# Kernel tuning notes

Hardware: AMD Instinct MI355X
Metric: run time of the kernel (lower is better)

Reference implementation:

```python
import jax, jax.numpy as jnp
import numpy as np

VMIN, VMAX, N = -5.0, 5.0, 100          # InvertiblePWL defaults
INT_LEN = (VMAX - VMIN) / (N - 1)       # bin width
B, D = 2_000_000, 16


def setup_inputs() -> dict:
    key = jax.random.key(0)
    k1, k2, k3, k4 = jax.random.split(key, 4)
    eps = jax.random.normal(k1, (B, D), dtype=jnp.float32)
    # small-magnitude adjacency so (I - A) is well-conditioned
    A = 0.05 * jax.random.normal(k2, (D, D), dtype=jnp.float32)
    # per-dim PWL params: torch inits p = randn(n+1)/5, b = randn(1) + vmin
    p = jax.random.normal(k3, (D, N + 1), dtype=jnp.float32) / 5.0
    b = jax.random.normal(k4, (D,), dtype=jnp.float32) + VMIN
    return {"eps": eps, "A": A, "p": p, "b": b}


def _pwl_forward(z, p, b):
    """Vectorized InvertiblePWL.forward over all d dims at once.
    z: [B, d]; p: [d, N+1]; b: [d]  ->  out: [B, d]
    """
    points = jnp.linspace(VMIN, VMAX, N, dtype=z.dtype)  # [N], same for all dims
    # delta_h is detached in torch (p[1:n] slice) -> stop_gradient
    delta_h = jax.lax.stop_gradient(INT_LEN * (jnp.exp(p[:, 1:N]) + 0.001))  # [d, N-1]
    # serial cumsum in torch == prefix-sum: delta_bias[0]=b, delta_bias[i+1]=delta_bias[i]+delta_h[i]
    delta_bias = b[:, None] + jnp.concatenate(
        [jnp.zeros((p.shape[0], 1), z.dtype), jnp.cumsum(delta_h, axis=1)], axis=1
    )  # [d, N]
    # index = sum(eps >= points) == searchsorted(points, z, 'right'), in [0, N]
    index = jnp.searchsorted(points, z, side="right")          # [B, d]
    sp_idx = jnp.maximum(index - 1, 0)                          # clamp at 0
    db = jnp.take_along_axis(delta_bias.T, sp_idx, axis=0)      # [B, d]
    sp = jax.lax.stop_gradient(points[sp_idx])                  # start points, detached
    w = jnp.exp(jnp.take_along_axis(p.T, index, axis=0)) + 0.001  # [B, d]
    return (z - sp) * w + db


def reference(eps, A, p, b):
    d = A.shape[0]
    # SCM.inv_cal: z = eps @ inv(I - A)
    adj_normalized = jnp.linalg.inv(jnp.eye(d, dtype=A.dtype) - A)
    z = eps @ adj_normalized                                    # [B, d]
    # SCM.prior_nlr: per-dim InvertiblePWL
    return _pwl_forward(z, p, b)
```

## Files before the change

kernel.cpp:

```cpp
#include <hip/hip_runtime.h>
#include <math.h>

#define D_DIM 16
#define N_PTS 100
#define VMIN_F (-5.0f)
#define INT_LEN_F (10.0f / 99.0f)
#define INV_INT_LEN_F (99.0f / 10.0f)

__global__ void scm_setup(const float* __restrict__ A,
                          const float* __restrict__ p,
                          const float* __restrict__ b,
                          float* __restrict__ Minv,
                          float* __restrict__ w_tab,
                          float* __restrict__ db) {
    __shared__ double aug[16][33];
    __shared__ int piv;
    const int t = threadIdx.x;

    if (t < 16) {
        #pragma unroll
        for (int j = 0; j < 16; j++) {
            aug[t][j]      = (t == j ? 1.0 : 0.0) - (double)A[t * 16 + j];
            aug[t][16 + j] = (t == j ? 1.0 : 0.0);
        }
    }
    __syncthreads();

    for (int k = 0; k < 16; k++) {
        if (t == 0) {
            int pr = k; double best = fabs(aug[k][k]);
            for (int i = k + 1; i < 16; i++) {
                double v = fabs(aug[i][k]);
                if (v > best) { best = v; pr = i; }
            }
            piv = pr;
        }
        __syncthreads();
        const int pr = piv;
        if (pr != k && t < 32) {
            double tmp = aug[k][t]; aug[k][t] = aug[pr][t]; aug[pr][t] = tmp;
        }
        __syncthreads();
        const double pivval = aug[k][k];
        __syncthreads();
        if (t < 32) aug[k][t] = aug[k][t] / pivval;
        __syncthreads();
        if (t < 16 && t != k) {
            const double f = aug[t][k];
            #pragma unroll
            for (int j = 0; j < 32; j++) aug[t][j] -= f * aug[k][j];
        }
        __syncthreads();
    }

    if (t < 16) {
        #pragma unroll
        for (int j = 0; j < 16; j++) Minv[t * 16 + j] = (float)aug[t][16 + j];
    }

    for (int i = t; i < 16 * (N_PTS + 1); i += blockDim.x)
        w_tab[i] = expf(p[i]) + 0.001f;

    if (t < 16) {
        float acc = b[t];
        db[t * N_PTS + 0] = acc;
        for (int i = 1; i < N_PTS; i++) {
            acc += INT_LEN_F * (expf(p[t * (N_PTS + 1) + i]) + 0.001f);
            db[t * N_PTS + i] = acc;
        }
    }
}

__global__ __launch_bounds__(256) void scm_main(
        const float* __restrict__ eps,
        const float* __restrict__ Minv,
        const float* __restrict__ w_tab,
        const float* __restrict__ db,
        float* __restrict__ out, int B) {
    __shared__ float sM[256];
    __shared__ float sW[16 * (N_PTS + 1)];
    __shared__ float sDB[16 * N_PTS];

    for (int i = threadIdx.x; i < 256; i += 256) sM[i] = Minv[i];
    for (int i = threadIdx.x; i < 16 * (N_PTS + 1); i += 256) sW[i] = w_tab[i];
    for (int i = threadIdx.x; i < 16 * N_PTS; i += 256) sDB[i] = db[i];
    __syncthreads();

    const int row = blockIdx.x * blockDim.x + threadIdx.x;
    if (row >= B) return;

    const float4* erow = (const float4*)(eps + (size_t)row * 16);
    float4 e0 = erow[0], e1 = erow[1], e2 = erow[2], e3 = erow[3];
    float e[16] = {e0.x, e0.y, e0.z, e0.w, e1.x, e1.y, e1.z, e1.w,
                   e2.x, e2.y, e2.z, e2.w, e3.x, e3.y, e3.z, e3.w};

    float z[16];
    #pragma unroll
    for (int d = 0; d < 16; d++) z[d] = 0.0f;

    #pragma unroll
    for (int k = 0; k < 16; k++) {
        const float ek = e[k];
        const float4 m0 = ((const float4*)sM)[k * 4 + 0];
        const float4 m1 = ((const float4*)sM)[k * 4 + 1];
        const float4 m2 = ((const float4*)sM)[k * 4 + 2];
        const float4 m3 = ((const float4*)sM)[k * 4 + 3];
        z[0]  = fmaf(ek, m0.x, z[0]);  z[1]  = fmaf(ek, m0.y, z[1]);
        z[2]  = fmaf(ek, m0.z, z[2]);  z[3]  = fmaf(ek, m0.w, z[3]);
        z[4]  = fmaf(ek, m1.x, z[4]);  z[5]  = fmaf(ek, m1.y, z[5]);
        z[6]  = fmaf(ek, m1.z, z[6]);  z[7]  = fmaf(ek, m1.w, z[7]);
        z[8]  = fmaf(ek, m2.x, z[8]);  z[9]  = fmaf(ek, m2.y, z[9]);
        z[10] = fmaf(ek, m2.z, z[10]); z[11] = fmaf(ek, m2.w, z[11]);
        z[12] = fmaf(ek, m3.x, z[12]); z[13] = fmaf(ek, m3.y, z[13]);
        z[14] = fmaf(ek, m3.z, z[14]); z[15] = fmaf(ek, m3.w, z[15]);
    }

    float o[16];
    #pragma unroll
    for (int d = 0; d < 16; d++) {
        const float zd = z[d];
        const float tt = (zd - VMIN_F) * INV_INT_LEN_F;
        int idx = (int)floorf(tt) + 1;
        idx = min(max(idx, 0), N_PTS);
        const int sp_idx = max(idx - 1, 0);
        const float sp = VMIN_F + (float)sp_idx * INT_LEN_F;
        const float w  = sW[d * (N_PTS + 1) + idx];
        const float dbv = sDB[d * N_PTS + sp_idx];
        o[d] = fmaf(zd - sp, w, dbv);
    }

    float4* orow = (float4*)(out + (size_t)row * 16);
    orow[0] = make_float4(o[0],  o[1],  o[2],  o[3]);
    orow[1] = make_float4(o[4],  o[5],  o[6],  o[7]);
    orow[2] = make_float4(o[8],  o[9],  o[10], o[11]);
    orow[3] = make_float4(o[12], o[13], o[14], o[15]);
}

extern "C" void kernel_launch(void* const* d_in, const int* in_sizes, int n_in,
                              void* d_out, int out_size, void* d_ws, size_t ws_size,
                              hipStream_t stream) {
    const float* eps = (const float*)d_in[0];
    const float* A   = (const float*)d_in[1];
    const float* p   = (const float*)d_in[2];
    const float* b   = (const float*)d_in[3];
    float* out = (float*)d_out;

    const int B = in_sizes[0] / D_DIM;

    float* ws    = (float*)d_ws;
    float* Minv  = ws;
    float* w_tab = ws + 256;
    float* db    = ws + 256 + 16 * (N_PTS + 1);

    scm_setup<<<1, 256, 0, stream>>>(A, p, b, Minv, w_tab, db);

    const int blocks = (B + 255) / 256;
    scm_main<<<blocks, 256, 0, stream>>>(eps, Minv, w_tab, db, out, B);
}
```

Baseline: 276.6 us.

## Stage eps rows and outputs through padded shared memory for coalesced access

Each block now loads its 256 rows of eps into shared memory with consecutive threads reading consecutive float4s. Rows are padded to five float4s to avoid bank conflicts, and the outputs are written back the same way. This replaces the per-thread 64-byte row accesses, which are strided across threads, with fully coalesced global loads and stores. The cost is 20 KB of extra LDS per block, which may lower occupancy, plus an extra barrier.

Result: slower. 307.0 us (+11.0%).

```diff
diff --git a/kernel.cpp b/kernel.cpp
--- a/kernel.cpp
+++ b/kernel.cpp
@@ -80,60 +80,85 @@
     __shared__ float sM[256];
     __shared__ float sW[16 * (N_PTS + 1)];
     __shared__ float sDB[16 * N_PTS];
+    __shared__ float4 sE[256 * 5];
 
-    for (int i = threadIdx.x; i < 256; i += 256) sM[i] = Minv[i];
-    for (int i = threadIdx.x; i < 16 * (N_PTS + 1); i += 256) sW[i] = w_tab[i];
-    for (int i = threadIdx.x; i < 16 * N_PTS; i += 256) sDB[i] = db[i];
+    const int t = threadIdx.x;
+
+    for (int i = t; i < 256; i += 256) sM[i] = Minv[i];
+    for (int i = t; i < 16 * (N_PTS + 1); i += 256) sW[i] = w_tab[i];
+    for (int i = t; i < 16 * N_PTS; i += 256) sDB[i] = db[i];
+
+    const int base = blockIdx.x * 256;
+    const int rows = min(256, B - base);
+
+    const float4* gin = (const float4*)(eps + (size_t)base * 16);
+    #pragma unroll
+    for (int q = 0; q < 4; q++) {
+        const int f = q * 256 + t;
+        if (f < rows * 4) {
+            sE[(f >> 2) * 5 + (f & 3)] = gin[f];
+        }
+    }
     __syncthreads();
 
-    const int row = blockIdx.x * blockDim.x + threadIdx.x;
-    if (row >= B) return;
+    if (t < rows) {
+        const float4 c0 = sE[t * 5 + 0];
+        const float4 c1 = sE[t * 5 + 1];
+        const float4 c2 = sE[t * 5 + 2];
+        const float4 c3 = sE[t * 5 + 3];
+        const float e[16] = {c0.x, c0.y, c0.z, c0.w, c1.x, c1.y, c1.z, c1.w,
+                             c2.x, c2.y, c2.z, c2.w, c3.x, c3.y, c3.z, c3.w};
 
-    const float4* erow = (const float4*)(eps + (size_t)row * 16);
-    float4 e0 = erow[0], e1 = erow[1], e2 = erow[2], e3 = erow[3];
-    float e[16] = {e0.x, e0.y, e0.z, e0.w, e1.x, e1.y, e1.z, e1.w,
-                   e2.x, e2.y, e2.z, e2.w, e3.x, e3.y, e3.z, e3.w};
+        float z[16];
+        #pragma unroll
+        for (int d = 0; d < 16; d++) z[d] = 0.0f;
 
-    float z[16];
+        #pragma unroll
+        for (int k = 0; k < 16; k++) {
+            const float ek = e[k];
+            const float4 m0 = ((const float4*)sM)[k * 4 + 0];
+            const float4 m1 = ((const float4*)sM)[k * 4 + 1];
+            const float4 m2 = ((const float4*)sM)[k * 4 + 2];
+            const float4 m3 = ((const float4*)sM)[k * 4 + 3];
+            z[0]  = fmaf(ek, m0.x, z[0]);  z[1]  = fmaf(ek, m0.y, z[1]);
+            z[2]  = fmaf(ek, m0.z, z[2]);  z[3]  = fmaf(ek, m0.w, z[3]);
+            z[4]  = fmaf(ek, m1.x, z[4]);  z[5]  = fmaf(ek, m1.y, z[5]);
+            z[6]  = fmaf(ek, m1.z, z[6]);  z[7]  = fmaf(ek, m1.w, z[7]);
+            z[8]  = fmaf(ek, m2.x, z[8]);  z[9]  = fmaf(ek, m2.y, z[9]);
+            z[10] = fmaf(ek, m2.z, z[10]); z[11] = fmaf(ek, m2.w, z[11]);
+            z[12] = fmaf(ek, m3.x, z[12]); z[13] = fmaf(ek, m3.y, z[13]);
+            z[14] = fmaf(ek, m3.z, z[14]); z[15] = fmaf(ek, m3.w, z[15]);
+        }
+
+        float o[16];
+        #pragma unroll
+        for (int d = 0; d < 16; d++) {
+            const float zd = z[d];
+            const float tt = (zd - VMIN_F) * INV_INT_LEN_F;
+            int idx = (int)floorf(tt) + 1;
+            idx = min(max(idx, 0), N_PTS);
+            const int sp_idx = max(idx - 1, 0);
+            const float sp = VMIN_F + (float)sp_idx * INT_LEN_F;
+            const float w  = sW[d * (N_PTS + 1) + idx];
+            const float dbv = sDB[d * N_PTS + sp_idx];
+            o[d] = fmaf(zd - sp, w, dbv);
+        }
+
+        sE[t * 5 + 0] = make_float4(o[0],  o[1],  o[2],  o[3]);
+        sE[t * 5 + 1] = make_float4(o[4],  o[5],  o[6],  o[7]);
+        sE[t * 5 + 2] = make_float4(o[8],  o[9],  o[10], o[11]);
+        sE[t * 5 + 3] = make_float4(o[12], o[13], o[14], o[15]);
+    }
+    __syncthreads();
+
+    float4* gout = (float4*)(out + (size_t)base * 16);
     #pragma unroll
-    for (int d = 0; d < 16; d++) z[d] = 0.0f;
-
-    #pragma unroll
-    for (int k = 0; k < 16; k++) {
-        const float ek = e[k];
-        const float4 m0 = ((const float4*)sM)[k * 4 + 0];
-        const float4 m1 = ((const float4*)sM)[k * 4 + 1];
-        const float4 m2 = ((const float4*)sM)[k * 4 + 2];
-        const float4 m3 = ((const float4*)sM)[k * 4 + 3];
-        z[0]  = fmaf(ek, m0.x, z[0]);  z[1]  = fmaf(ek, m0.y, z[1]);
-        z[2]  = fmaf(ek, m0.z, z[2]);  z[3]  = fmaf(ek, m0.w, z[3]);
-        z[4]  = fmaf(ek, m1.x, z[4]);  z[5]  = fmaf(ek, m1.y, z[5]);
-        z[6]  = fmaf(ek, m1.z, z[6]);  z[7]  = fmaf(ek, m1.w, z[7]);
-        z[8]  = fmaf(ek, m2.x, z[8]);  z[9]  = fmaf(ek, m2.y, z[9]);
-        z[10] = fmaf(ek, m2.z, z[10]); z[11] = fmaf(ek, m2.w, z[11]);
-        z[12] = fmaf(ek, m3.x, z[12]); z[13] = fmaf(ek, m3.y, z[13]);
-        z[14] = fmaf(ek, m3.z, z[14]); z[15] = fmaf(ek, m3.w, z[15]);
+    for (int q = 0; q < 4; q++) {
+        const int f = q * 256 + t;
+        if (f < rows * 4) {
+            gout[f] = sE[(f >> 2) * 5 + (f & 3)];
+        }
     }
-
-    float o[16];
-    #pragma unroll
-    for (int d = 0; d < 16; d++) {
-        const float zd = z[d];
-        const float tt = (zd - VMIN_F) * INV_INT_LEN_F;
-        int idx = (int)floorf(tt) + 1;
-        idx = min(max(idx, 0), N_PTS);
-        const int sp_idx = max(idx - 1, 0);
-        const float sp = VMIN_F + (float)sp_idx * INT_LEN_F;
-        const float w  = sW[d * (N_PTS + 1) + idx];
-        const float dbv = sDB[d * N_PTS + sp_idx];
-        o[d] = fmaf(zd - sp, w, dbv);
-    }
-
-    float4* orow = (float4*)(out + (size_t)row * 16);
-    orow[0] = make_float4(o[0],  o[1],  o[2],  o[3]);
-    orow[1] = make_float4(o[4],  o[5],  o[6],  o[7]);
-    orow[2] = make_float4(o[8],  o[9],  o[10], o[11]);
-    orow[3] = make_float4(o[12], o[13], o[14], o[15]);
 }
 
 extern "C" void kernel_launch(void* const* d_in, const int* in_sizes, int n_in,
```

## Interleave PWL weight and bias into float2 table and read Minv uniformly

Applied to the files above, without the earlier changes.

The setup kernel now writes one float2 table per (dim, index) entry that holds the slope and the matching cumulative bias, so the main kernel does one 8-byte LDS read per output instead of two separate lookups. Minv is no longer staged in shared memory. It is read straight from global memory with uniform addresses, which should become scalar loads and cuts the shared-memory fill and the per-k LDS reads. The eps row loads are issued before the shared-memory fill and barrier so global latency overlaps the table staging. Costs are a larger shared table in bytes and a dependence on the scalar cache for Minv.

New measurement: 285.9 us. 1.03x slower.

```diff
diff --git a/kernel.cpp b/kernel.cpp
--- a/kernel.cpp
+++ b/kernel.cpp
@@ -11,9 +11,9 @@
                           const float* __restrict__ p,
                           const float* __restrict__ b,
                           float* __restrict__ Minv,
-                          float* __restrict__ w_tab,
-                          float* __restrict__ db) {
+                          float2* __restrict__ Ctab) {
     __shared__ double aug[16][33];
+    __shared__ float db_s[16][N_PTS];
     __shared__ int piv;
     const int t = threadIdx.x;
 
@@ -58,41 +58,50 @@
         for (int j = 0; j < 16; j++) Minv[t * 16 + j] = (float)aug[t][16 + j];
     }
 
-    for (int i = t; i < 16 * (N_PTS + 1); i += blockDim.x)
-        w_tab[i] = expf(p[i]) + 0.001f;
-
     if (t < 16) {
         float acc = b[t];
-        db[t * N_PTS + 0] = acc;
+        db_s[t][0] = acc;
         for (int i = 1; i < N_PTS; i++) {
             acc += INT_LEN_F * (expf(p[t * (N_PTS + 1) + i]) + 0.001f);
-            db[t * N_PTS + i] = acc;
+            db_s[t][i] = acc;
         }
+    }
+    __syncthreads();
+
+    for (int i = t; i < 16 * (N_PTS + 1); i += blockDim.x) {
+        const int d   = i / (N_PTS + 1);
+        const int idx = i - d * (N_PTS + 1);
+        const int spi = idx > 0 ? idx - 1 : 0;
+        float2 c;
+        c.x = expf(p[i]) + 0.001f;
+        c.y = db_s[d][spi];
+        Ctab[i] = c;
     }
 }
 
 __global__ __launch_bounds__(256) void scm_main(
         const float* __restrict__ eps,
         const float* __restrict__ Minv,
-        const float* __restrict__ w_tab,
-        const float* __restrict__ db,
+        const float2* __restrict__ Ctab,
         float* __restrict__ out, int B) {
-    __shared__ float sM[256];
-    __shared__ float sW[16 * (N_PTS + 1)];
-    __shared__ float sDB[16 * N_PTS];
+    __shared__ float2 sC[16 * (N_PTS + 1)];
 
-    for (int i = threadIdx.x; i < 256; i += 256) sM[i] = Minv[i];
-    for (int i = threadIdx.x; i < 16 * (N_PTS + 1); i += 256) sW[i] = w_tab[i];
-    for (int i = threadIdx.x; i < 16 * N_PTS; i += 256) sDB[i] = db[i];
+    const int t = threadIdx.x;
+    const int row = blockIdx.x * 256 + t;
+
+    float4 c0 = {0,0,0,0}, c1 = {0,0,0,0}, c2 = {0,0,0,0}, c3 = {0,0,0,0};
+    if (row < B) {
+        const float4* erow = (const float4*)(eps + (size_t)row * 16);
+        c0 = erow[0]; c1 = erow[1]; c2 = erow[2]; c3 = erow[3];
+    }
+
+    for (int i = t; i < 16 * (N_PTS + 1); i += 256) sC[i] = Ctab[i];
     __syncthreads();
 
-    const int row = blockIdx.x * blockDim.x + threadIdx.x;
     if (row >= B) return;
 
-    const float4* erow = (const float4*)(eps + (size_t)row * 16);
-    float4 e0 = erow[0], e1 = erow[1], e2 = erow[2], e3 = erow[3];
-    float e[16] = {e0.x, e0.y, e0.z, e0.w, e1.x, e1.y, e1.z, e1.w,
-                   e2.x, e2.y, e2.z, e2.w, e3.x, e3.y, e3.z, e3.w};
+    const float e[16] = {c0.x, c0.y, c0.z, c0.w, c1.x, c1.y, c1.z, c1.w,
+                         c2.x, c2.y, c2.z, c2.w, c3.x, c3.y, c3.z, c3.w};
 
     float z[16];
     #pragma unroll
@@ -101,18 +110,10 @@
     #pragma unroll
     for (int k = 0; k < 16; k++) {
         const float ek = e[k];
-        const float4 m0 = ((const float4*)sM)[k * 4 + 0];
-        const float4 m1 = ((const float4*)sM)[k * 4 + 1];
-        const float4 m2 = ((const float4*)sM)[k * 4 + 2];
-        const float4 m3 = ((const float4*)sM)[k * 4 + 3];
-        z[0]  = fmaf(ek, m0.x, z[0]);  z[1]  = fmaf(ek, m0.y, z[1]);
-        z[2]  = fmaf(ek, m0.z, z[2]);  z[3]  = fmaf(ek, m0.w, z[3]);
-        z[4]  = fmaf(ek, m1.x, z[4]);  z[5]  = fmaf(ek, m1.y, z[5]);
-        z[6]  = fmaf(ek, m1.z, z[6]);  z[7]  = fmaf(ek, m1.w, z[7]);
-        z[8]  = fmaf(ek, m2.x, z[8]);  z[9]  = fmaf(ek, m2.y, z[9]);
-        z[10] = fmaf(ek, m2.z, z[10]); z[11] = fmaf(ek, m2.w, z[11]);
-        z[12] = fmaf(ek, m3.x, z[12]); z[13] = fmaf(ek, m3.y, z[13]);
-        z[14] = fmaf(ek, m3.z, z[14]); z[15] = fmaf(ek, m3.w, z[15]);
+        #pragma unroll
+        for (int d = 0; d < 16; d++) {
+            z[d] = fmaf(ek, Minv[k * 16 + d], z[d]);
+        }
     }
 
     float o[16];
@@ -124,9 +125,8 @@
         idx = min(max(idx, 0), N_PTS);
         const int sp_idx = max(idx - 1, 0);
         const float sp = VMIN_F + (float)sp_idx * INT_LEN_F;
-        const float w  = sW[d * (N_PTS + 1) + idx];
-        const float dbv = sDB[d * N_PTS + sp_idx];
-        o[d] = fmaf(zd - sp, w, dbv);
+        const float2 c = sC[d * (N_PTS + 1) + idx];
+        o[d] = fmaf(zd - sp, c.x, c.y);
     }
 
     float4* orow = (float4*)(out + (size_t)row * 16);
@@ -147,13 +147,12 @@
 
     const int B = in_sizes[0] / D_DIM;
 
-    float* ws    = (float*)d_ws;
-    float* Minv  = ws;
-    float* w_tab = ws + 256;
-    float* db    = ws + 256 + 16 * (N_PTS + 1);
+    float*  ws   = (float*)d_ws;
+    float*  Minv = ws;
+    float2* Ctab = (float2*)(ws + 256);
 
-    scm_setup<<<1, 256, 0, stream>>>(A, p, b, Minv, w_tab, db);
+    scm_setup<<<1, 256, 0, stream>>>(A, p, b, Minv, Ctab);
 
     const int blocks = (B + 255) / 256;
-    scm_main<<<blocks, 256, 0, stream>>>(eps, Minv, w_tab, db, out, B);
+    scm_main<<<blocks, 256, 0, stream>>>(eps, Minv, Ctab, out, B);
 }
```
